# Optimization experiments

Measured on AMD Instinct MI355X. Metric: run time of the kernel, lower is better.

## Reference

```python
import jax, jax.numpy as jnp
import numpy as np

B, H, S, D = 4, 16, 2048, 64

def setup_inputs() -> dict:
    key = jax.random.key(0)
    kq, kk, kv = jax.random.split(key, 3)
    return {
        "input_query": jax.random.normal(kq, (B, H, S, D), dtype=jnp.float32),
        "input_key": jax.random.normal(kk, (B, H, S, D), dtype=jnp.float32),
        "input_value": jax.random.normal(kv, (B, H, S, D), dtype=jnp.float32),
    }

def reference(input_query, input_key, input_value):
    # Unscaled, unmasked attention: softmax(Q K^T) V
    scores = jnp.einsum("bhsd,bhtd->bhst", input_query, input_key)  # [B,H,S,S]
    probs = jax.nn.softmax(scores, axis=-1)
    return jnp.einsum("bhst,bhtd->bhsd", probs, input_value)  # [B,H,S,D]
```

## Files before the change

kernel.cpp:

```cpp
#include <hip/hip_runtime.h>
#include <hip/hip_bf16.h>
#include <stdint.h>

#define SEQ 2048
#define DIM 64
#define NH  64
#define KT  32
#define NT  (SEQ / KT)
#define RAW_BYTES  16384
#define FRAG_BYTES 12288
#define KF_BYTES   8192

typedef __attribute__((ext_vector_type(8)))  short    bf16x8;
typedef __attribute__((ext_vector_type(8)))  _Float16 f16x8;
typedef __attribute__((ext_vector_type(16))) float    f32x16;
typedef unsigned int u32;

#if __has_builtin(__builtin_amdgcn_exp2f)
#define EXP2(x) __builtin_amdgcn_exp2f(x)
#else
#define EXP2(x) exp2f(x)
#endif

__device__ __forceinline__ int phi(int s) {
    int h = (s >> 2) & 1, b = s >> 3, i = s & 3;
    return 8 * h + 4 * b + i + (b >= 2 ? 8 : 0);
}
__device__ __forceinline__ short f2bf(float f) {
    union { float f; u32 u; } v; v.f = f;
    u32 r = v.u + 0x7fffu + ((v.u >> 16) & 1u);
    return (short)(r >> 16);
}

__device__ __forceinline__ void stage_tile(const float* gK, const float* gV,
                                           char* raw, int wave, int lane) {
    const int P  = wave * 64 + lane;
    const int sk = (P & ~15) | ((P & 15) ^ ((P >> 4) & 7));
    char* dK = raw + (size_t)(wave * 64) * 16;
    char* dV = raw + 8192 + (size_t)(wave * 64) * 16;
    __builtin_amdgcn_global_load_lds(
        (const __attribute__((address_space(1))) u32*)((const char*)gK + (size_t)sk * 16),
        (__attribute__((address_space(3))) u32*)dK, 16, 0, 0);
    __builtin_amdgcn_global_load_lds(
        (const __attribute__((address_space(1))) u32*)((const char*)gV + (size_t)P * 16),
        (__attribute__((address_space(3))) u32*)dV, 16, 0, 0);
}

__device__ __forceinline__ void convert_tile(const char* raw, char* frag, int t) {
    const int lane = t & 63, col = lane & 31, h = lane >> 5;
    if (t < 256) {
        const int c = t >> 6;
        const int r = phi(col);
        const int kk = 4 * c + 2 * h;
        const float4* rk = (const float4*)raw;
        float4 a = rk[r * 16 + ((kk    ) ^ (r & 7))];
        float4 b = rk[r * 16 + ((kk + 1) ^ (r & 7))];
        float x[8] = {a.x, a.y, a.z, a.w, b.x, b.y, b.z, b.w};
        f16x8 hi, lo;
        #pragma unroll
        for (int j = 0; j < 8; ++j) {
            _Float16 xh = (_Float16)x[j];
            hi[j] = xh;
            lo[j] = (_Float16)(x[j] - (float)xh);
        }
        *(f16x8*)(frag + (c * 2 + 0) * 1024 + lane * 16) = hi;
        *(f16x8*)(frag + (c * 2 + 1) * 1024 + lane * 16) = lo;
    } else {
        const int u = t - 256;
        const int f = u >> 7, c = (u >> 6) & 1;
        const float* rv = (const float*)(raw + 8192);
        bf16x8 v;
        #pragma unroll
        for (int j = 0; j < 8; ++j) {
            int key = phi(16 * c + 8 * h + j);
            v[j] = f2bf(rv[key * 64 + f * 32 + col]);
        }
        *(bf16x8*)(frag + KF_BYTES + (f * 2 + c) * 1024 + lane * 16) = v;
    }
}

__global__ __launch_bounds__(512, 4) void attn_fused(
    const float* __restrict__ Q, const float* __restrict__ K,
    const float* __restrict__ V, float* __restrict__ O)
{
    __shared__ __align__(16) char raw[3][RAW_BYTES];
    __shared__ __align__(16) char frag[2][FRAG_BYTES];

    const int tid  = threadIdx.x;
    const int wave = tid >> 6, lane = tid & 63;
    const int h = lane >> 5, col = lane & 31;

    const int bid  = blockIdx.x;
    const int head = (bid & 7) * 8 + ((bid >> 3) & 7);
    const int qw   = (bid >> 6) * 256 + wave * 32;
    const size_t base = (size_t)head * SEQ * DIM;
    const float* Kh = K + base;
    const float* Vh = V + base;

    f16x8 qf[4];
    {
        const float* qr = Q + base + (size_t)(qw + col) * DIM;
        #pragma unroll
        for (int c = 0; c < 4; ++c)
            #pragma unroll
            for (int j = 0; j < 8; ++j)
                qf[c][j] = (_Float16)(qr[c * 16 + 8 * h + j] * 1.44269504088896f);
    }

    f32x16 z16;
    #pragma unroll
    for (int r = 0; r < 16; ++r) z16[r] = 0.f;
    f32x16 of[2];
    of[0] = z16; of[1] = z16;
    float l_own = 0.f;

    stage_tile(Kh, Vh, raw[0], wave, lane);
    stage_tile(Kh + KT * DIM, Vh + KT * DIM, raw[1], wave, lane);
    asm volatile("s_waitcnt vmcnt(2)" ::: "memory");
    __builtin_amdgcn_s_barrier();
    __builtin_amdgcn_sched_barrier(0);
    convert_tile(raw[0], frag[0], tid);

    int stg_i = 2;
    int cvt_i = 1;

    for (int kt = 0; kt < NT; ++kt) {
        asm volatile("s_waitcnt lgkmcnt(0)" ::: "memory");
        __builtin_amdgcn_s_barrier();
        __builtin_amdgcn_sched_barrier(0);

        if (kt + 2 < NT)
            stage_tile(Kh + (size_t)(kt + 2) * KT * DIM,
                       Vh + (size_t)(kt + 2) * KT * DIM, raw[stg_i], wave, lane);
        const char* cur = frag[kt & 1];

        f32x16 s = z16;
        __builtin_amdgcn_s_setprio(1);
        #pragma unroll
        for (int c = 0; c < 4; ++c) {
            f16x8 kh = *(const f16x8*)(cur + (c * 2 + 0) * 1024 + lane * 16);
            f16x8 kl = *(const f16x8*)(cur + (c * 2 + 1) * 1024 + lane * 16);
            s = __builtin_amdgcn_mfma_f32_32x32x16_f16(kh, qf[c], s, 0, 0, 0);
            s = __builtin_amdgcn_mfma_f32_32x32x16_f16(kl, qf[c], s, 0, 0, 0);
        }
        __builtin_amdgcn_s_setprio(0);

        bf16x8 pfrag[2];
        {
            float p[16], ls = 0.f;
            #pragma unroll
            for (int r = 0; r < 16; ++r) { p[r] = EXP2(s[r]); ls += p[r]; }
            l_own += ls;
            u32 pk[8], sw[8];
            #pragma unroll
            for (int m = 0; m < 8; ++m) {
                __hip_bfloat162 b2 = __float22bfloat162_rn(make_float2(p[2 * m], p[2 * m + 1]));
                __builtin_memcpy(&pk[m], &b2, 4);
            }
            #pragma unroll
            for (int m = 0; m < 8; ++m) sw[m] = __shfl_xor(pk[m], 32);
            #pragma unroll
            for (int c = 0; c < 2; ++c) {
                union { u32 w[4]; bf16x8 v; } fr;
                fr.w[0] = h ? sw[4 * c + 2] : pk[4 * c + 0];
                fr.w[1] = h ? sw[4 * c + 3] : pk[4 * c + 1];
                fr.w[2] = h ? pk[4 * c + 2] : sw[4 * c + 0];
                fr.w[3] = h ? pk[4 * c + 3] : sw[4 * c + 1];
                pfrag[c] = fr.v;
            }
        }

        __builtin_amdgcn_s_setprio(1);
        #pragma unroll
        for (int f = 0; f < 2; ++f)
            #pragma unroll
            for (int c = 0; c < 2; ++c) {
                bf16x8 vf = *(const bf16x8*)(cur + KF_BYTES + (f * 2 + c) * 1024 + lane * 16);
                of[f] = __builtin_amdgcn_mfma_f32_32x32x16_bf16(pfrag[c], vf, of[f], 0, 0, 0);
            }
        __builtin_amdgcn_s_setprio(0);

        if (kt + 1 < NT) {
            if (kt + 2 < NT) asm volatile("s_waitcnt vmcnt(2)" ::: "memory");
            else             asm volatile("s_waitcnt vmcnt(0)" ::: "memory");
            __builtin_amdgcn_s_barrier();
            __builtin_amdgcn_sched_barrier(0);
            convert_tile(raw[cvt_i], frag[(kt + 1) & 1], tid);
        }
        stg_i = (stg_i == 2) ? 0 : stg_i + 1;
        cvt_i = (cvt_i == 2) ? 0 : cvt_i + 1;
    }

    float* op = O + base;
    {
        float lall = l_own + __shfl_xor(l_own, 32);
        float inv = 1.0f / lall;
        #pragma unroll
        for (int r = 0; r < 16; ++r) {
            int qrow = (r & 3) + 8 * (r >> 2) + 4 * h;
            float iq = __shfl(inv, qrow);
            op[(size_t)(qw + qrow) * DIM + col]      = of[0][r] * iq;
            op[(size_t)(qw + qrow) * DIM + 32 + col] = of[1][r] * iq;
        }
    }
}

extern "C" void kernel_launch(void* const* d_in, const int* in_sizes, int n_in,
                              void* d_out, int out_size, void* d_ws, size_t ws_size,
                              hipStream_t stream) {
    const float* Q = (const float*)d_in[0];
    const float* K = (const float*)d_in[1];
    const float* V = (const float*)d_in[2];
    float* Out = (float*)d_out;
    (void)d_ws; (void)ws_size;

    attn_fused<<<dim3(NH * (SEQ / 256)), dim3(512), 0, stream>>>(Q, K, V, Out);
}
```

Before: 231.8 us.

## Split block into compute and producer waves for K/V staging and conversion

Adds four producer waves per block that stage K through LDS, load V directly into registers, and convert both into fp16/bf16 fragments in a triple-buffered ring. The eight compute waves now only run the MFMA and softmax work and no longer do the conversion themselves. The aim is to take staging and conversion latency off the compute critical path through warp specialisation. In exchange, blocks grow to 768 threads with a higher launch-bounds occupancy target, which may limit registers. The uncoalesced strided V register loads and the shared barrier scheme between the two wave groups also add risk.

```diff
diff --git a/kernel.cpp b/kernel.cpp
--- a/kernel.cpp
+++ b/kernel.cpp
@@ -7,12 +7,13 @@
 #define NH  64
 #define KT  32
 #define NT  (SEQ / KT)
-#define RAW_BYTES  16384
+#define RAWK_BYTES 8192
 #define FRAG_BYTES 12288
 #define KF_BYTES   8192
 
 typedef __attribute__((ext_vector_type(8)))  short    bf16x8;
 typedef __attribute__((ext_vector_type(8)))  _Float16 f16x8;
+typedef __attribute__((ext_vector_type(8)))  float    f32x8;
 typedef __attribute__((ext_vector_type(16))) float    f32x16;
 typedef unsigned int u32;
 
@@ -32,59 +33,12 @@
     return (short)(r >> 16);
 }
 
-__device__ __forceinline__ void stage_tile(const float* gK, const float* gV,
-                                           char* raw, int wave, int lane) {
-    const int P  = wave * 64 + lane;
-    const int sk = (P & ~15) | ((P & 15) ^ ((P >> 4) & 7));
-    char* dK = raw + (size_t)(wave * 64) * 16;
-    char* dV = raw + 8192 + (size_t)(wave * 64) * 16;
-    __builtin_amdgcn_global_load_lds(
-        (const __attribute__((address_space(1))) u32*)((const char*)gK + (size_t)sk * 16),
-        (__attribute__((address_space(3))) u32*)dK, 16, 0, 0);
-    __builtin_amdgcn_global_load_lds(
-        (const __attribute__((address_space(1))) u32*)((const char*)gV + (size_t)P * 16),
-        (__attribute__((address_space(3))) u32*)dV, 16, 0, 0);
-}
-
-__device__ __forceinline__ void convert_tile(const char* raw, char* frag, int t) {
-    const int lane = t & 63, col = lane & 31, h = lane >> 5;
-    if (t < 256) {
-        const int c = t >> 6;
-        const int r = phi(col);
-        const int kk = 4 * c + 2 * h;
-        const float4* rk = (const float4*)raw;
-        float4 a = rk[r * 16 + ((kk    ) ^ (r & 7))];
-        float4 b = rk[r * 16 + ((kk + 1) ^ (r & 7))];
-        float x[8] = {a.x, a.y, a.z, a.w, b.x, b.y, b.z, b.w};
-        f16x8 hi, lo;
-        #pragma unroll
-        for (int j = 0; j < 8; ++j) {
-            _Float16 xh = (_Float16)x[j];
-            hi[j] = xh;
-            lo[j] = (_Float16)(x[j] - (float)xh);
-        }
-        *(f16x8*)(frag + (c * 2 + 0) * 1024 + lane * 16) = hi;
-        *(f16x8*)(frag + (c * 2 + 1) * 1024 + lane * 16) = lo;
-    } else {
-        const int u = t - 256;
-        const int f = u >> 7, c = (u >> 6) & 1;
-        const float* rv = (const float*)(raw + 8192);
-        bf16x8 v;
-        #pragma unroll
-        for (int j = 0; j < 8; ++j) {
-            int key = phi(16 * c + 8 * h + j);
-            v[j] = f2bf(rv[key * 64 + f * 32 + col]);
-        }
-        *(bf16x8*)(frag + KF_BYTES + (f * 2 + c) * 1024 + lane * 16) = v;
-    }
-}
-
-__global__ __launch_bounds__(512, 4) void attn_fused(
+__global__ __launch_bounds__(768, 6) void attn_fused(
     const float* __restrict__ Q, const float* __restrict__ K,
     const float* __restrict__ V, float* __restrict__ O)
 {
-    __shared__ __align__(16) char raw[3][RAW_BYTES];
-    __shared__ __align__(16) char frag[2][FRAG_BYTES];
+    __shared__ __align__(16) char rawK[3][RAWK_BYTES];
+    __shared__ __align__(16) char frag[3][FRAG_BYTES];
 
     const int tid  = threadIdx.x;
     const int wave = tid >> 6, lane = tid & 63;
@@ -92,115 +46,176 @@
 
     const int bid  = blockIdx.x;
     const int head = (bid & 7) * 8 + ((bid >> 3) & 7);
-    const int qw   = (bid >> 6) * 256 + wave * 32;
     const size_t base = (size_t)head * SEQ * DIM;
-    const float* Kh = K + base;
-    const float* Vh = V + base;
-
-    f16x8 qf[4];
-    {
-        const float* qr = Q + base + (size_t)(qw + col) * DIM;
+
+    if (wave < 8) {
+        const int qw = (bid >> 6) * 256 + wave * 32;
+
+        f16x8 qf[4];
+        {
+            const float* qr = Q + base + (size_t)(qw + col) * DIM;
+            #pragma unroll
+            for (int c = 0; c < 4; ++c)
+                #pragma unroll
+                for (int j = 0; j < 8; ++j)
+                    qf[c][j] = (_Float16)(qr[c * 16 + 8 * h + j] * 1.44269504088896f);
+        }
+
+        f32x16 z16;
         #pragma unroll
-        for (int c = 0; c < 4; ++c)
-            #pragma unroll
-            for (int j = 0; j < 8; ++j)
-                qf[c][j] = (_Float16)(qr[c * 16 + 8 * h + j] * 1.44269504088896f);
-    }
-
-    f32x16 z16;
-    #pragma unroll
-    for (int r = 0; r < 16; ++r) z16[r] = 0.f;
-    f32x16 of[2];
-    of[0] = z16; of[1] = z16;
-    float l_own = 0.f;
-
-    stage_tile(Kh, Vh, raw[0], wave, lane);
-    stage_tile(Kh + KT * DIM, Vh + KT * DIM, raw[1], wave, lane);
-    asm volatile("s_waitcnt vmcnt(2)" ::: "memory");
-    __builtin_amdgcn_s_barrier();
-    __builtin_amdgcn_sched_barrier(0);
-    convert_tile(raw[0], frag[0], tid);
-
-    int stg_i = 2;
-    int cvt_i = 1;
-
-    for (int kt = 0; kt < NT; ++kt) {
-        asm volatile("s_waitcnt lgkmcnt(0)" ::: "memory");
+        for (int r = 0; r < 16; ++r) z16[r] = 0.f;
+        f32x16 of[2];
+        of[0] = z16; of[1] = z16;
+        float l_own = 0.f;
+
         __builtin_amdgcn_s_barrier();
-        __builtin_amdgcn_sched_barrier(0);
-
-        if (kt + 2 < NT)
-            stage_tile(Kh + (size_t)(kt + 2) * KT * DIM,
-                       Vh + (size_t)(kt + 2) * KT * DIM, raw[stg_i], wave, lane);
-        const char* cur = frag[kt & 1];
-
-        f32x16 s = z16;
-        __builtin_amdgcn_s_setprio(1);
-        #pragma unroll
-        for (int c = 0; c < 4; ++c) {
-            f16x8 kh = *(const f16x8*)(cur + (c * 2 + 0) * 1024 + lane * 16);
-            f16x8 kl = *(const f16x8*)(cur + (c * 2 + 1) * 1024 + lane * 16);
-            s = __builtin_amdgcn_mfma_f32_32x32x16_f16(kh, qf[c], s, 0, 0, 0);
-            s = __builtin_amdgcn_mfma_f32_32x32x16_f16(kl, qf[c], s, 0, 0, 0);
-        }
-        __builtin_amdgcn_s_setprio(0);
-
-        bf16x8 pfrag[2];
-        {
-            float p[16], ls = 0.f;
-            #pragma unroll
-            for (int r = 0; r < 16; ++r) { p[r] = EXP2(s[r]); ls += p[r]; }
-            l_own += ls;
-            u32 pk[8], sw[8];
-            #pragma unroll
-            for (int m = 0; m < 8; ++m) {
-                __hip_bfloat162 b2 = __float22bfloat162_rn(make_float2(p[2 * m], p[2 * m + 1]));
-                __builtin_memcpy(&pk[m], &b2, 4);
-            }
-            #pragma unroll
-            for (int m = 0; m < 8; ++m) sw[m] = __shfl_xor(pk[m], 32);
-            #pragma unroll
-            for (int c = 0; c < 2; ++c) {
-                union { u32 w[4]; bf16x8 v; } fr;
-                fr.w[0] = h ? sw[4 * c + 2] : pk[4 * c + 0];
-                fr.w[1] = h ? sw[4 * c + 3] : pk[4 * c + 1];
-                fr.w[2] = h ? pk[4 * c + 2] : sw[4 * c + 0];
-                fr.w[3] = h ? pk[4 * c + 3] : sw[4 * c + 1];
-                pfrag[c] = fr.v;
-            }
-        }
-
-        __builtin_amdgcn_s_setprio(1);
-        #pragma unroll
-        for (int f = 0; f < 2; ++f)
-            #pragma unroll
-            for (int c = 0; c < 2; ++c) {
-                bf16x8 vf = *(const bf16x8*)(cur + KF_BYTES + (f * 2 + c) * 1024 + lane * 16);
-                of[f] = __builtin_amdgcn_mfma_f32_32x32x16_bf16(pfrag[c], vf, of[f], 0, 0, 0);
-            }
-        __builtin_amdgcn_s_setprio(0);
-
-        if (kt + 1 < NT) {
-            if (kt + 2 < NT) asm volatile("s_waitcnt vmcnt(2)" ::: "memory");
-            else             asm volatile("s_waitcnt vmcnt(0)" ::: "memory");
+
+        int fi = 0;
+        for (int kt = 0; kt < NT; ++kt) {
+            asm volatile("s_waitcnt lgkmcnt(0)" ::: "memory");
             __builtin_amdgcn_s_barrier();
             __builtin_amdgcn_sched_barrier(0);
-            convert_tile(raw[cvt_i], frag[(kt + 1) & 1], tid);
-        }
-        stg_i = (stg_i == 2) ? 0 : stg_i + 1;
-        cvt_i = (cvt_i == 2) ? 0 : cvt_i + 1;
-    }
-
-    float* op = O + base;
-    {
-        float lall = l_own + __shfl_xor(l_own, 32);
-        float inv = 1.0f / lall;
+            const char* cur = frag[fi];
+
+            f32x16 s = z16;
+            __builtin_amdgcn_s_setprio(1);
+            #pragma unroll
+            for (int c = 0; c < 4; ++c) {
+                f16x8 kh = *(const f16x8*)(cur + (c * 2 + 0) * 1024 + lane * 16);
+                f16x8 kl = *(const f16x8*)(cur + (c * 2 + 1) * 1024 + lane * 16);
+                s = __builtin_amdgcn_mfma_f32_32x32x16_f16(kh, qf[c], s, 0, 0, 0);
+                s = __builtin_amdgcn_mfma_f32_32x32x16_f16(kl, qf[c], s, 0, 0, 0);
+            }
+            __builtin_amdgcn_s_setprio(0);
+
+            bf16x8 pfrag[2];
+            {
+                float p[16], ls = 0.f;
+                #pragma unroll
+                for (int r = 0; r < 16; ++r) { p[r] = EXP2(s[r]); ls += p[r]; }
+                l_own += ls;
+                u32 pk[8], sw[8];
+                #pragma unroll
+                for (int m = 0; m < 8; ++m) {
+                    __hip_bfloat162 b2 = __float22bfloat162_rn(make_float2(p[2 * m], p[2 * m + 1]));
+                    __builtin_memcpy(&pk[m], &b2, 4);
+                }
+                #pragma unroll
+                for (int m = 0; m < 8; ++m) sw[m] = __shfl_xor(pk[m], 32);
+                #pragma unroll
+                for (int c = 0; c < 2; ++c) {
+                    union { u32 w[4]; bf16x8 v; } fr;
+                    fr.w[0] = h ? sw[4 * c + 2] : pk[4 * c + 0];
+                    fr.w[1] = h ? sw[4 * c + 3] : pk[4 * c + 1];
+                    fr.w[2] = h ? pk[4 * c + 2] : sw[4 * c + 0];
+                    fr.w[3] = h ? pk[4 * c + 3] : sw[4 * c + 1];
+                    pfrag[c] = fr.v;
+                }
+            }
+
+            __builtin_amdgcn_s_setprio(1);
+            #pragma unroll
+            for (int f = 0; f < 2; ++f)
+                #pragma unroll
+                for (int c = 0; c < 2; ++c) {
+                    bf16x8 vf = *(const bf16x8*)(cur + KF_BYTES + (f * 2 + c) * 1024 + lane * 16);
+                    of[f] = __builtin_amdgcn_mfma_f32_32x32x16_bf16(pfrag[c], vf, of[f], 0, 0, 0);
+                }
+            __builtin_amdgcn_s_setprio(0);
+
+            fi = (fi == 2) ? 0 : fi + 1;
+        }
+
+        float* op = O + base;
+        {
+            float lall = l_own + __shfl_xor(l_own, 32);
+            float inv = 1.0f / lall;
+            #pragma unroll
+            for (int r = 0; r < 16; ++r) {
+                int qrow = (r & 3) + 8 * (r >> 2) + 4 * h;
+                float iq = __shfl(inv, qrow);
+                op[(size_t)(qw + qrow) * DIM + col]      = of[0][r] * iq;
+                op[(size_t)(qw + qrow) * DIM + 32 + col] = of[1][r] * iq;
+            }
+        }
+    } else {
+        const int pw = wave - 8;
+        const float* Kh = K + base;
+        const float* Vh = V + base;
+
+        const int fv = pw >> 1, cv = pw & 1;
+        int vrow[8];
         #pragma unroll
-        for (int r = 0; r < 16; ++r) {
-            int qrow = (r & 3) + 8 * (r >> 2) + 4 * h;
-            float iq = __shfl(inv, qrow);
-            op[(size_t)(qw + qrow) * DIM + col]      = of[0][r] * iq;
-            op[(size_t)(qw + qrow) * DIM + 32 + col] = of[1][r] * iq;
+        for (int j = 0; j < 8; ++j) vrow[j] = phi(16 * cv + 8 * h + j);
+
+        auto stageK = [&](int kt, char* dst) {
+            const char* g = (const char*)(Kh + (size_t)kt * (KT * DIM));
+            #pragma unroll
+            for (int i = 0; i < 2; ++i) {
+                const int P  = pw * 128 + i * 64 + lane;
+                const int sk = (P & ~15) | ((P & 15) ^ ((P >> 4) & 7));
+                char* d = dst + (size_t)(pw * 128 + i * 64) * 16;
+                __builtin_amdgcn_global_load_lds(
+                    (const __attribute__((address_space(1))) u32*)(g + (size_t)sk * 16),
+                    (__attribute__((address_space(3))) u32*)d, 16, 0, 0);
+            }
+        };
+        auto loadV = [&](int kt) -> f32x8 {
+            const float* vp = Vh + (size_t)kt * (KT * DIM) + fv * 32 + col;
+            f32x8 r;
+            #pragma unroll
+            for (int j = 0; j < 8; ++j) r[j] = vp[vrow[j] * DIM];
+            return r;
+        };
+        auto convert = [&](const char* rk_, char* fr, f32x8 vv) {
+            const int r = phi(col);
+            const int kk = 4 * pw + 2 * h;
+            const float4* rk4 = (const float4*)rk_;
+            float4 a = rk4[r * 16 + ((kk    ) ^ (r & 7))];
+            float4 b = rk4[r * 16 + ((kk + 1) ^ (r & 7))];
+            float x[8] = {a.x, a.y, a.z, a.w, b.x, b.y, b.z, b.w};
+            f16x8 hi, lo;
+            #pragma unroll
+            for (int j = 0; j < 8; ++j) {
+                _Float16 xh = (_Float16)x[j];
+                hi[j] = xh;
+                lo[j] = (_Float16)(x[j] - (float)xh);
+            }
+            *(f16x8*)(fr + (pw * 2 + 0) * 1024 + lane * 16) = hi;
+            *(f16x8*)(fr + (pw * 2 + 1) * 1024 + lane * 16) = lo;
+            bf16x8 v;
+            #pragma unroll
+            for (int j = 0; j < 8; ++j) v[j] = f2bf(vv[j]);
+            *(bf16x8*)(fr + KF_BYTES + (fv * 2 + cv) * 1024 + lane * 16) = v;
+        };
+
+        stageK(0, rawK[0]);
+        stageK(1, rawK[1]);
+        f32x8 vvA = loadV(0);
+        f32x8 vvB = loadV(1);
+        asm volatile("s_waitcnt vmcnt(0)" ::: "memory");
+        __builtin_amdgcn_s_barrier();
+        convert(rawK[0], frag[0], vvA);
+        convert(rawK[1], frag[1], vvB);
+        stageK(2, rawK[2]);
+        vvA = loadV(2);
+
+        int ri = 2, si = 0;
+        for (int kt = 0; kt < NT; ++kt) {
+            asm volatile("s_waitcnt vmcnt(0) lgkmcnt(0)" ::: "memory");
+            __builtin_amdgcn_s_barrier();
+            __builtin_amdgcn_sched_barrier(0);
+
+            const bool ld = (kt + 3 < NT);
+            if (ld) stageK(kt + 3, rawK[si]);
+            f32x8 vnext;
+            if (ld) vnext = loadV(kt + 3);
+            if (kt + 2 < NT)
+                convert(rawK[ri], frag[ri], (kt & 1) ? vvB : vvA);
+            if (ld) { if (kt & 1) vvA = vnext; else vvB = vnext; }
+
+            ri = (ri == 2) ? 0 : ri + 1;
+            si = (si == 2) ? 0 : si + 1;
         }
     }
 }
@@ -214,5 +229,5 @@
     float* Out = (float*)d_out;
     (void)d_ws; (void)ws_size;
 
-    attn_fused<<<dim3(NH * (SEQ / 256)), dim3(512), 0, stream>>>(Q, K, V, Out);
-}
+    attn_fused<<<dim3(NH * (SEQ / 256)), dim3(768), 0, stream>>>(Q, K, V, Out);
+}
```

Measured after the change: 235.2 us. Within noise of the previous version (+1.5%).
